# Kernel optimization log

Measured on AMD Instinct MI355X. Metric: run time of the kernel, lower is better.

Reference implementation:

```python
import jax, jax.numpy as jnp
import numpy as np

B, C, W, H = 32, 256, 64, 64
CQ = C // 4

def setup_inputs() -> dict:
    key = jax.random.key(0)
    ks = jax.random.split(key, 9)
    s = lambda fan: 1.0 / np.sqrt(fan)
    return {
        "x_0": jax.random.normal(ks[0], (B, C, W, H), jnp.float32),
        "x_1": jax.random.normal(ks[1], (B, C, W, H), jnp.float32),
        "Wq": jax.random.normal(ks[2], (CQ, C), jnp.float32) * s(C),
        "bq": jax.random.normal(ks[3], (CQ,), jnp.float32) * 0.01,
        "Wk": jax.random.normal(ks[4], (CQ, C), jnp.float32) * s(C),
        "bk": jax.random.normal(ks[5], (CQ,), jnp.float32) * 0.01,
        "Wv": jax.random.normal(ks[6], (C, C), jnp.float32) * s(C),
        "bv": jax.random.normal(ks[7], (C,), jnp.float32) * 0.01,
        "gamma": jax.random.normal(ks[8], (1,), jnp.float32) * 0.1,
    }

def reference(x_0, x_1, Wq, bq, Wk, bk, Wv, bv, gamma):
    # 1x1 convs == channel GEMMs
    q = jnp.einsum('oc,bchw->bohw', Wq, x_0) + bq[None, :, None, None]  # [B, C/4, W, H]
    k = jnp.einsum('oc,bchw->bohw', Wk, x_1) + bk[None, :, None, None]  # [B, C/4, W, H]
    v = jnp.einsum('oc,bchw->bohw', Wv, x_0) + bv[None, :, None, None]  # [B, C, W, H]
    b0 = x_0.shape[0]
    b1, c1, w1, h1 = x_1.shape
    proj_query = q.reshape(b0, -1).T            # [D, B0], D = (C/4)*W*H
    proj_key = k.reshape(b1, -1)                # [B1, D]
    energy = proj_key @ proj_query              # [B1, B0] attention over BATCH axis
    attention = jax.nn.softmax(energy, axis=-1)
    proj_value = v.reshape(b0, -1)              # [B0, C*W*H]
    out = (attention @ proj_value).reshape(b1, c1, w1, h1)
    out = gamma[0] * out + x_1
    return out, attention
```

## Files before the change

### kernel.cpp

```cpp
#include <hip/hip_runtime.h>

#define NB  32
#define NC  256
#define NCQ 64
#define WHT 4096
#define DQK ((size_t)NCQ * WHT)
#define MV  ((size_t)NC * WHT)

typedef __attribute__((ext_vector_type(8))) short short8;
typedef __attribute__((ext_vector_type(4))) float f32x4;
typedef __attribute__((ext_vector_type(2))) float f32x2;
typedef unsigned short ushort_t;

__device__ __forceinline__ ushort_t bf16_rne(float f) {
    union { float f; unsigned u; } v; v.f = f;
    unsigned r = (v.u + 0x7fffu + ((v.u >> 16) & 1u)) >> 16;
    return (ushort_t)r;
}
__device__ __forceinline__ float bf16_f(ushort_t h) {
    union { unsigned u; float f; } v; v.u = ((unsigned)h) << 16; return v.f;
}

__device__ __forceinline__ int frag_off(int r, int kk) {
    return ((kk >> 5) * 16 + ((kk >> 3) & 3) * 4 + (r >> 4)) * 128
           + (r & 15) * 8 + (kk & 7);
}

__global__ __launch_bounds__(256)
void prep_w(const float* __restrict__ Wq, const float* __restrict__ Wk,
            const float* __restrict__ Wv,
            ushort_t* __restrict__ wv_hi,
            ushort_t* __restrict__ wq_hi, ushort_t* __restrict__ wq_lo,
            ushort_t* __restrict__ wk_hi, ushort_t* __restrict__ wk_lo)
{
    int i = blockIdx.x * 256 + threadIdx.x;
    if (i < 65536) {
        int R = i >> 8, kk = i & 255;
        wv_hi[(R >> 6) * 16384 + frag_off(R & 63, kk)] = bf16_rne(Wv[i]);
    } else if (i < 81920) {
        int j = i - 65536; int r = j >> 8, kk = j & 255;
        float f = Wq[j]; ushort_t h = bf16_rne(f);
        int o = frag_off(r, kk);
        wq_hi[o] = h; wq_lo[o] = bf16_rne(f - bf16_f(h));
    } else if (i < 98304) {
        int j = i - 81920; int r = j >> 8, kk = j & 255;
        float f = Wk[j]; ushort_t h = bf16_rne(f);
        int o = frag_off(r, kk);
        wk_hi[o] = h; wk_lo[o] = bf16_rne(f - bf16_f(h));
    }
}

#define LOADB(dst, kbv) do {                                            \
    const float* xk_ = xw + (size_t)(kbv) * 32 * WHT;                   \
    _Pragma("unroll") for (int n_ = 0; n_ < 2; ++n_)                    \
    _Pragma("unroll") for (int e_ = 0; e_ < 8; ++e_)                    \
        dst[n_][e_] = xk_[(size_t)e_ * WHT + n_ * 16];                  \
} while (0)

__global__ __launch_bounds__(512, 4)
void qkv_mfma(const float* __restrict__ x0, const float* __restrict__ x1,
              const ushort_t* __restrict__ wv_hi,
              const ushort_t* __restrict__ wq_hi, const ushort_t* __restrict__ wq_lo,
              const ushort_t* __restrict__ wk_hi, const ushort_t* __restrict__ wk_lo,
              const float* __restrict__ bq, const float* __restrict__ bk,
              const float* __restrict__ bv,
              float* __restrict__ q, float* __restrict__ k,
              ushort_t* __restrict__ vbf)
{
    __shared__ ushort_t lds_hi[16384];
    __shared__ ushort_t lds_lo[16384];

    const int t   = threadIdx.x;
    const int bid = blockIdx.x;
    const int xcd = bid & 7;
    const int sl  = bid >> 3;
    const int mt  = sl % 6;
    const int g   = (sl / 6) * 8 + xcd;
    const int nt  = g & 15;
    const int b   = g >> 4;

    const bool isV = (mt < 4);
    const bool isQ = (mt == 4);

    const int wave = t >> 6;
    const int lane = t & 63;
    const int lh   = lane >> 4;
    const int ll   = lane & 15;

    const ushort_t* whi = isV ? (wv_hi + mt * 16384) : (isQ ? wq_hi : wk_hi);
    const ushort_t* wlo = isQ ? wq_lo : wk_lo;

#pragma unroll
    for (int r = 0; r < 4; ++r)
        *(short8*)&lds_hi[(r * 512 + t) * 8] = *(const short8*)(whi + (r * 512 + t) * 8);
    if (!isV) {
#pragma unroll
        for (int r = 0; r < 4; ++r)
            *(short8*)&lds_lo[(r * 512 + t) * 8] = *(const short8*)(wlo + (r * 512 + t) * 8);
    }
    __syncthreads();

    const float* xw = ((mt == 5) ? x1 : x0) + (size_t)b * NC * WHT
                      + nt * 256 + wave * 32 + ll + (size_t)lh * 8 * WHT;
    const int abase = lh * 512 + ll * 8;

    f32x4 acc[4][2];
#pragma unroll
    for (int m = 0; m < 4; ++m)
#pragma unroll
        for (int n = 0; n < 2; ++n) acc[m][n] = (f32x4){0.f, 0.f, 0.f, 0.f};

    float xfA[2][8], xfB[2][8];
    LOADB(xfA, 0);

#pragma unroll
    for (int kb = 0; kb < 8; ++kb) {
        float (*cur)[8] = (kb & 1) ? xfB : xfA;
        float (*nxt)[8] = (kb & 1) ? xfA : xfB;
        if (kb < 7) LOADB(nxt, kb + 1);

        short8 bh[2];
#pragma unroll
        for (int n = 0; n < 2; ++n) {
            union { unsigned u[4]; short8 s; } pk;
#pragma unroll
            for (int p = 0; p < 4; ++p)
                pk.u[p] = __builtin_amdgcn_perm(
                    __float_as_uint(cur[n][2 * p + 1]),
                    __float_as_uint(cur[n][2 * p]), 0x07060302u);
            bh[n] = pk.s;
        }

        if (isV) {
#pragma unroll
            for (int m = 0; m < 4; ++m) {
                short8 a_hi = *(const short8*)&lds_hi[kb * 2048 + abase + m * 128];
#pragma unroll
                for (int n = 0; n < 2; ++n)
                    acc[m][n] = __builtin_amdgcn_mfma_f32_16x16x32_bf16(
                        a_hi, bh[n], acc[m][n], 0, 0, 0);
            }
        } else {
            short8 bl[2];
#pragma unroll
            for (int n = 0; n < 2; ++n) {
                float lo[8];
#pragma unroll
                for (int e = 0; e < 8; ++e) {
                    float hf = __uint_as_float(__float_as_uint(cur[n][e]) & 0xffff0000u);
                    lo[e] = cur[n][e] - hf;
                }
                union { unsigned u[4]; short8 s; } pk;
#pragma unroll
                for (int p = 0; p < 4; ++p)
                    pk.u[p] = __builtin_amdgcn_perm(
                        __float_as_uint(lo[2 * p + 1]),
                        __float_as_uint(lo[2 * p]), 0x07060302u);
                bl[n] = pk.s;
            }
#pragma unroll
            for (int m = 0; m < 4; ++m) {
                short8 a_hi = *(const short8*)&lds_hi[kb * 2048 + abase + m * 128];
                short8 a_lo = *(const short8*)&lds_lo[kb * 2048 + abase + m * 128];
#pragma unroll
                for (int n = 0; n < 2; ++n) {
                    acc[m][n] = __builtin_amdgcn_mfma_f32_16x16x32_bf16(
                        a_hi, bh[n], acc[m][n], 0, 0, 0);
                    acc[m][n] = __builtin_amdgcn_mfma_f32_16x16x32_bf16(
                        a_hi, bl[n], acc[m][n], 0, 0, 0);
                    acc[m][n] = __builtin_amdgcn_mfma_f32_16x16x32_bf16(
                        a_lo, bh[n], acc[m][n], 0, 0, 0);
                }
            }
        }
    }

    const int colbase = nt * 256 + wave * 32;
    if (isV) {
        ushort_t* outp = vbf + ((size_t)b * NC + mt * 64) * WHT + colbase;
        const float* bias = bv + mt * 64;
#pragma unroll
        for (int m = 0; m < 4; ++m)
#pragma unroll
            for (int n = 0; n < 2; ++n)
#pragma unroll
                for (int r = 0; r < 4; ++r) {
                    const int row = m * 16 + 4 * lh + r;
                    outp[(size_t)row * WHT + n * 16 + ll] =
                        bf16_rne(acc[m][n][r] + bias[row]);
                }
    } else {
        float* outp = (isQ ? q : k) + (size_t)b * NCQ * WHT + colbase;
        const float* bias = isQ ? bq : bk;
#pragma unroll
        for (int m = 0; m < 4; ++m)
#pragma unroll
            for (int n = 0; n < 2; ++n)
#pragma unroll
                for (int r = 0; r < 4; ++r) {
                    const int row = m * 16 + 4 * lh + r;
                    outp[(size_t)row * WHT + n * 16 + ll] =
                        acc[m][n][r] + bias[row];
                }
    }
}

__global__ __launch_bounds__(256)
void energy_kernel(const float* __restrict__ q, const float* __restrict__ k,
                   float* __restrict__ energy)
{
    __shared__ float kt[256][17];
    __shared__ float qt[256][17];

    const int t  = threadIdx.x;
    const int d0 = blockIdx.x * 256;
    const int ih = blockIdx.y;
    const int jh = blockIdx.z;

    for (int r = 0; r < 16; ++r) {
        kt[t][r] = k[(size_t)(ih * 16 + r) * DQK + d0 + t];
        qt[t][r] = q[(size_t)(jh * 16 + r) * DQK + d0 + t];
    }
    __syncthreads();

    const int ii = t >> 4;
    const int jj = t & 15;
    float a0 = 0.f, a1 = 0.f, a2 = 0.f, a3 = 0.f;
#pragma unroll 8
    for (int d = 0; d < 256; d += 4) {
        a0 = fmaf(kt[d + 0][ii], qt[d + 0][jj], a0);
        a1 = fmaf(kt[d + 1][ii], qt[d + 1][jj], a1);
        a2 = fmaf(kt[d + 2][ii], qt[d + 2][jj], a2);
        a3 = fmaf(kt[d + 3][ii], qt[d + 3][jj], a3);
    }

    atomicAdd(&energy[(ih * 16 + ii) * 32 + jh * 16 + jj], (a0 + a1) + (a2 + a3));
}

__global__ __launch_bounds__(1024)
void softmax_kernel(const float* __restrict__ energy,
                    float* __restrict__ att, float* __restrict__ att_out)
{
    const int t = threadIdx.x;
    const int i = t >> 5;
    const int j = t & 31;
    float e = energy[i * 32 + j];
    float m = e;
#pragma unroll
    for (int o = 16; o; o >>= 1) m = fmaxf(m, __shfl_xor(m, o, 32));
    float ex = __expf(e - m);
    float s = ex;
#pragma unroll
    for (int o = 16; o; o >>= 1) s += __shfl_xor(s, o, 32);
    float a = ex / s;
    att[i * 32 + j] = a;
    att_out[i * 32 + j] = a;
}

__global__ __launch_bounds__(256)
void out_kernel(const ushort_t* __restrict__ vbf, const float* __restrict__ att,
                const float* __restrict__ x1, const float* __restrict__ gamma,
                float* __restrict__ out)
{
    const int t = threadIdx.x;
    const size_t m0 = (size_t)blockIdx.x * 512 + 2 * t;

    float v0[32], v1[32];
#pragma unroll
    for (int j = 0; j < 32; ++j) {
        unsigned u = *(const unsigned*)(vbf + (size_t)j * MV + m0);
        v0[j] = __uint_as_float(u << 16);
        v1[j] = __uint_as_float(u & 0xffff0000u);
    }

    const float g = gamma[0];
    for (int i = 0; i < 32; ++i) {
        float a0 = 0.f, a1 = 0.f;
#pragma unroll
        for (int j = 0; j < 32; ++j) {
            float w = att[i * 32 + j];
            a0 = fmaf(w, v0[j], a0);
            a1 = fmaf(w, v1[j], a1);
        }
        f32x2 xx = *(const f32x2*)(x1 + (size_t)i * MV + m0);
        f32x2 oo; oo.x = g * a0 + xx.x; oo.y = g * a1 + xx.y;
        *(f32x2*)(out + (size_t)i * MV + m0) = oo;
    }
}

extern "C" void kernel_launch(void* const* d_in, const int* in_sizes, int n_in,
                              void* d_out, int out_size, void* d_ws, size_t ws_size,
                              hipStream_t stream)
{
    const float* x0    = (const float*)d_in[0];
    const float* x1    = (const float*)d_in[1];
    const float* Wq    = (const float*)d_in[2];
    const float* bq    = (const float*)d_in[3];
    const float* Wk    = (const float*)d_in[4];
    const float* bk    = (const float*)d_in[5];
    const float* Wv    = (const float*)d_in[6];
    const float* bv    = (const float*)d_in[7];
    const float* gamma = (const float*)d_in[8];

    float* ws     = (float*)d_ws;
    float* q      = ws;
    float* k      = q + (size_t)NB * NCQ * WHT;
    float* energy = k + (size_t)NB * NCQ * WHT;
    float* att    = energy + 1024;

    ushort_t* wv_hi = (ushort_t*)(att + 1024);
    ushort_t* wq_hi = wv_hi + 65536;
    ushort_t* wq_lo = wq_hi + 16384;
    ushort_t* wk_hi = wq_lo + 16384;
    ushort_t* wk_lo = wk_hi + 16384;
    ushort_t* vbf   = wk_lo + 16384;

    float* out     = (float*)d_out;
    float* att_out = out + (size_t)NB * NC * WHT;

    hipMemsetAsync(energy, 0, 1024 * sizeof(float), stream);

    prep_w<<<384, 256, 0, stream>>>(Wq, Wk, Wv, wv_hi, wq_hi, wq_lo, wk_hi, wk_lo);
    qkv_mfma<<<3072, 512, 0, stream>>>(x0, x1, wv_hi, wq_hi, wq_lo, wk_hi, wk_lo,
                                       bq, bk, bv, q, k, vbf);
    energy_kernel<<<dim3(1024, 2, 2), 256, 0, stream>>>(q, k, energy);
    softmax_kernel<<<1, 1024, 0, stream>>>(energy, att, att_out);
    out_kernel<<<2048, 256, 0, stream>>>(vbf, att, x1, gamma, out);
}
```

Baseline: 246.0 us.

## Split Q/K projection blocks in half, drop lo LDS, add explicit pipelining

Q and K tiles were the slow blocks because each does three MFMAs per product on the same work as a V tile. This change splits each Q and K tile across two blocks handling 128 columns each, which raises the grid from 3072 to 4096 blocks and balances per-block work. The lo weight fragments are now read straight from global memory instead of a second LDS buffer, which halves LDS use. The double-buffered loads are restructured with sched_barriers to control interleaving. The risks are extra global traffic for the lo weights and more block launches.

```diff
diff --git a/kernel.cpp b/kernel.cpp
--- a/kernel.cpp
+++ b/kernel.cpp
@@ -50,12 +50,59 @@
     }
 }
 
-#define LOADB(dst, kbv) do {                                            \
+#define PACK_HI(dst, src) do {                                          \
+    union { unsigned u[4]; short8 s; } pk_;                             \
+    _Pragma("unroll") for (int p_ = 0; p_ < 4; ++p_)                    \
+        pk_.u[p_] = __builtin_amdgcn_perm(                              \
+            __float_as_uint(src[2 * p_ + 1]),                           \
+            __float_as_uint(src[2 * p_]), 0x07060302u);                 \
+    dst = pk_.s;                                                        \
+} while (0)
+
+#define LOADB2(dst, kbv) do {                                           \
     const float* xk_ = xw + (size_t)(kbv) * 32 * WHT;                   \
     _Pragma("unroll") for (int n_ = 0; n_ < 2; ++n_)                    \
     _Pragma("unroll") for (int e_ = 0; e_ < 8; ++e_)                    \
         dst[n_][e_] = xk_[(size_t)e_ * WHT + n_ * 16];                  \
 } while (0)
+
+#define LOADB1(dst, kbv) do {                                           \
+    const float* xk_ = xw + (size_t)(kbv) * 32 * WHT;                   \
+    _Pragma("unroll") for (int e_ = 0; e_ < 8; ++e_)                    \
+        dst[e_] = xk_[(size_t)e_ * WHT];                                \
+} while (0)
+
+#define PROCV(buf, kbv) do {                                            \
+    short8 bh_[2];                                                      \
+    _Pragma("unroll") for (int n_ = 0; n_ < 2; ++n_)                    \
+        PACK_HI(bh_[n_], buf[n_]);                                      \
+    _Pragma("unroll") for (int m_ = 0; m_ < 4; ++m_) {                  \
+        short8 ah_ = *(const short8*)&lds_hi[(kbv) * 2048 + abase + m_ * 128]; \
+        _Pragma("unroll") for (int n_ = 0; n_ < 2; ++n_)                \
+            acc[m_][n_] = __builtin_amdgcn_mfma_f32_16x16x32_bf16(      \
+                ah_, bh_[n_], acc[m_][n_], 0, 0, 0);                    \
+    }                                                                   \
+} while (0)
+
+#define PROCQK(buf, kbv) do {                                           \
+    short8 bh_, bl_;                                                    \
+    PACK_HI(bh_, buf);                                                  \
+    float lo_[8];                                                       \
+    _Pragma("unroll") for (int e_ = 0; e_ < 8; ++e_) {                  \
+        float hf_ = __uint_as_float(__float_as_uint(buf[e_]) & 0xffff0000u); \
+        lo_[e_] = buf[e_] - hf_;                                        \
+    }                                                                   \
+    PACK_HI(bl_, lo_);                                                  \
+    _Pragma("unroll") for (int m_ = 0; m_ < 4; ++m_) {                  \
+        short8 ah_ = *(const short8*)&lds_hi[(kbv) * 2048 + abase + m_ * 128]; \
+        short8 al_ = *(const short8*)(wlo + (kbv) * 2048 + abase + m_ * 128);  \
+        acc2[m_] = __builtin_amdgcn_mfma_f32_16x16x32_bf16(ah_, bh_, acc2[m_], 0, 0, 0); \
+        acc2[m_] = __builtin_amdgcn_mfma_f32_16x16x32_bf16(ah_, bl_, acc2[m_], 0, 0, 0); \
+        acc2[m_] = __builtin_amdgcn_mfma_f32_16x16x32_bf16(al_, bh_, acc2[m_], 0, 0, 0); \
+    }                                                                   \
+} while (0)
+
+#define SBAR() __builtin_amdgcn_sched_barrier(0)
 
 __global__ __launch_bounds__(512, 4)
 void qkv_mfma(const float* __restrict__ x0, const float* __restrict__ x1,
@@ -68,117 +115,61 @@
               ushort_t* __restrict__ vbf)
 {
     __shared__ ushort_t lds_hi[16384];
-    __shared__ ushort_t lds_lo[16384];
 
     const int t   = threadIdx.x;
     const int bid = blockIdx.x;
-    const int xcd = bid & 7;
-    const int sl  = bid >> 3;
-    const int mt  = sl % 6;
-    const int g   = (sl / 6) * 8 + xcd;
-    const int nt  = g & 15;
-    const int b   = g >> 4;
-
-    const bool isV = (mt < 4);
-    const bool isQ = (mt == 4);
+    const int xcd  = bid & 7;
+    const int r0   = bid >> 3;
+    const int slot = r0 & 7;
+    const int gg   = r0 >> 3;
+    const int g    = gg * 8 + xcd;
+    const int nt   = g & 15;
+    const int b    = g >> 4;
+
+    const bool isV = (slot < 4);
 
     const int wave = t >> 6;
     const int lane = t & 63;
     const int lh   = lane >> 4;
     const int ll   = lane & 15;
 
-    const ushort_t* whi = isV ? (wv_hi + mt * 16384) : (isQ ? wq_hi : wk_hi);
-    const ushort_t* wlo = isQ ? wq_lo : wk_lo;
+    const ushort_t* whi = isV ? (wv_hi + slot * 16384)
+                              : ((slot < 6) ? wq_hi : wk_hi);
 
 #pragma unroll
     for (int r = 0; r < 4; ++r)
         *(short8*)&lds_hi[(r * 512 + t) * 8] = *(const short8*)(whi + (r * 512 + t) * 8);
-    if (!isV) {
-#pragma unroll
-        for (int r = 0; r < 4; ++r)
-            *(short8*)&lds_lo[(r * 512 + t) * 8] = *(const short8*)(wlo + (r * 512 + t) * 8);
-    }
     __syncthreads();
 
-    const float* xw = ((mt == 5) ? x1 : x0) + (size_t)b * NC * WHT
-                      + nt * 256 + wave * 32 + ll + (size_t)lh * 8 * WHT;
     const int abase = lh * 512 + ll * 8;
 
-    f32x4 acc[4][2];
-#pragma unroll
-    for (int m = 0; m < 4; ++m)
-#pragma unroll
-        for (int n = 0; n < 2; ++n) acc[m][n] = (f32x4){0.f, 0.f, 0.f, 0.f};
-
-    float xfA[2][8], xfB[2][8];
-    LOADB(xfA, 0);
-
-#pragma unroll
-    for (int kb = 0; kb < 8; ++kb) {
-        float (*cur)[8] = (kb & 1) ? xfB : xfA;
-        float (*nxt)[8] = (kb & 1) ? xfA : xfB;
-        if (kb < 7) LOADB(nxt, kb + 1);
-
-        short8 bh[2];
-#pragma unroll
-        for (int n = 0; n < 2; ++n) {
-            union { unsigned u[4]; short8 s; } pk;
-#pragma unroll
-            for (int p = 0; p < 4; ++p)
-                pk.u[p] = __builtin_amdgcn_perm(
-                    __float_as_uint(cur[n][2 * p + 1]),
-                    __float_as_uint(cur[n][2 * p]), 0x07060302u);
-            bh[n] = pk.s;
+    if (isV) {
+        const float* xw = x0 + (size_t)b * NC * WHT
+                          + nt * 256 + wave * 32 + ll + (size_t)lh * 8 * WHT;
+
+        f32x4 acc[4][2];
+#pragma unroll
+        for (int m = 0; m < 4; ++m)
+#pragma unroll
+            for (int n = 0; n < 2; ++n) acc[m][n] = (f32x4){0.f, 0.f, 0.f, 0.f};
+
+        float xfA[2][8], xfB[2][8];
+        LOADB2(xfA, 0);
+        SBAR();
+#pragma unroll
+        for (int p = 0; p < 4; ++p) {
+            LOADB2(xfB, 2 * p + 1);
+            SBAR();
+            PROCV(xfA, 2 * p);
+            if (p < 3) LOADB2(xfA, 2 * p + 2);
+            SBAR();
+            PROCV(xfB, 2 * p + 1);
+            SBAR();
         }
 
-        if (isV) {
-#pragma unroll
-            for (int m = 0; m < 4; ++m) {
-                short8 a_hi = *(const short8*)&lds_hi[kb * 2048 + abase + m * 128];
-#pragma unroll
-                for (int n = 0; n < 2; ++n)
-                    acc[m][n] = __builtin_amdgcn_mfma_f32_16x16x32_bf16(
-                        a_hi, bh[n], acc[m][n], 0, 0, 0);
-            }
-        } else {
-            short8 bl[2];
-#pragma unroll
-            for (int n = 0; n < 2; ++n) {
-                float lo[8];
-#pragma unroll
-                for (int e = 0; e < 8; ++e) {
-                    float hf = __uint_as_float(__float_as_uint(cur[n][e]) & 0xffff0000u);
-                    lo[e] = cur[n][e] - hf;
-                }
-                union { unsigned u[4]; short8 s; } pk;
-#pragma unroll
-                for (int p = 0; p < 4; ++p)
-                    pk.u[p] = __builtin_amdgcn_perm(
-                        __float_as_uint(lo[2 * p + 1]),
-                        __float_as_uint(lo[2 * p]), 0x07060302u);
-                bl[n] = pk.s;
-            }
-#pragma unroll
-            for (int m = 0; m < 4; ++m) {
-                short8 a_hi = *(const short8*)&lds_hi[kb * 2048 + abase + m * 128];
-                short8 a_lo = *(const short8*)&lds_lo[kb * 2048 + abase + m * 128];
-#pragma unroll
-                for (int n = 0; n < 2; ++n) {
-                    acc[m][n] = __builtin_amdgcn_mfma_f32_16x16x32_bf16(
-                        a_hi, bh[n], acc[m][n], 0, 0, 0);
-                    acc[m][n] = __builtin_amdgcn_mfma_f32_16x16x32_bf16(
-                        a_hi, bl[n], acc[m][n], 0, 0, 0);
-                    acc[m][n] = __builtin_amdgcn_mfma_f32_16x16x32_bf16(
-                        a_lo, bh[n], acc[m][n], 0, 0, 0);
-                }
-            }
-        }
-    }
-
-    const int colbase = nt * 256 + wave * 32;
-    if (isV) {
-        ushort_t* outp = vbf + ((size_t)b * NC + mt * 64) * WHT + colbase;
-        const float* bias = bv + mt * 64;
+        const int colbase = nt * 256 + wave * 32;
+        ushort_t* outp = vbf + ((size_t)b * NC + slot * 64) * WHT + colbase;
+        const float* bias = bv + slot * 64;
 #pragma unroll
         for (int m = 0; m < 4; ++m)
 #pragma unroll
@@ -190,18 +181,42 @@
                         bf16_rne(acc[m][n][r] + bias[row]);
                 }
     } else {
+        const bool isQ  = (slot < 6);
+        const int  half = slot & 1;
+        const ushort_t* wlo = isQ ? wq_lo : wk_lo;
+
+        const float* xw = (isQ ? x0 : x1) + (size_t)b * NC * WHT
+                          + nt * 256 + half * 128 + wave * 16 + ll
+                          + (size_t)lh * 8 * WHT;
+
+        f32x4 acc2[4];
+#pragma unroll
+        for (int m = 0; m < 4; ++m) acc2[m] = (f32x4){0.f, 0.f, 0.f, 0.f};
+
+        float xfA[8], xfB[8];
+        LOADB1(xfA, 0);
+        SBAR();
+#pragma unroll
+        for (int p = 0; p < 4; ++p) {
+            LOADB1(xfB, 2 * p + 1);
+            SBAR();
+            PROCQK(xfA, 2 * p);
+            if (p < 3) LOADB1(xfA, 2 * p + 2);
+            SBAR();
+            PROCQK(xfB, 2 * p + 1);
+            SBAR();
+        }
+
+        const int colbase = nt * 256 + half * 128 + wave * 16;
         float* outp = (isQ ? q : k) + (size_t)b * NCQ * WHT + colbase;
         const float* bias = isQ ? bq : bk;
 #pragma unroll
         for (int m = 0; m < 4; ++m)
 #pragma unroll
-            for (int n = 0; n < 2; ++n)
-#pragma unroll
-                for (int r = 0; r < 4; ++r) {
-                    const int row = m * 16 + 4 * lh + r;
-                    outp[(size_t)row * WHT + n * 16 + ll] =
-                        acc[m][n][r] + bias[row];
-                }
+            for (int r = 0; r < 4; ++r) {
+                const int row = m * 16 + 4 * lh + r;
+                outp[(size_t)row * WHT + ll] = acc2[m][r] + bias[row];
+            }
     }
 }
 
@@ -321,7 +336,7 @@
     hipMemsetAsync(energy, 0, 1024 * sizeof(float), stream);
 
     prep_w<<<384, 256, 0, stream>>>(Wq, Wk, Wv, wv_hi, wq_hi, wq_lo, wk_hi, wk_lo);
-    qkv_mfma<<<3072, 512, 0, stream>>>(x0, x1, wv_hi, wq_hi, wq_lo, wk_hi, wk_lo,
+    qkv_mfma<<<4096, 512, 0, stream>>>(x0, x1, wv_hi, wq_hi, wq_lo, wk_hi, wk_lo,
                                        bq, bk, bv, q, k, vbf);
     energy_kernel<<<dim3(1024, 2, 2), 256, 0, stream>>>(q, k, energy);
     softmax_kernel<<<1, 1024, 0, stream>>>(energy, att, att_out);
```

Measured after the change: 264.3 us. +7.4%, slower.

## Stage X panels via global_load_lds and fuse softmax into output kernel

Applied to the files above, without the earlier changes.

The QKV projection kernel now streams activation panels into double-buffered LDS with asynchronous global-to-LDS loads and reads the bf16 weight fragments straight from global memory, where before the weights sat in LDS and activations went direct to registers. This is meant to coalesce the strided activation reads and overlap them with MFMA work, at the cost of a barrier per k-step and uncached weight loads from global. Separately, the single-block softmax kernel is removed: every output block recomputes the 32x32 softmax into shared memory and block 0 writes the attention output, saving a launch and a round trip through global memory in exchange for redundant softmax work.

```diff
diff --git a/kernel.cpp b/kernel.cpp
--- a/kernel.cpp
+++ b/kernel.cpp
@@ -24,6 +24,12 @@
 __device__ __forceinline__ int frag_off(int r, int kk) {
     return ((kk >> 5) * 16 + ((kk >> 3) & 3) * 4 + (r >> 4)) * 128
            + (r & 15) * 8 + (kk & 7);
+}
+
+__device__ __forceinline__ void gload_lds16(const float* g, float* l) {
+    __builtin_amdgcn_global_load_lds(
+        (const __attribute__((address_space(1))) unsigned*)g,
+        (__attribute__((address_space(3))) unsigned*)l, 16, 0, 0);
 }
 
 __global__ __launch_bounds__(256)
@@ -50,11 +56,27 @@
     }
 }
 
-#define LOADB(dst, kbv) do {                                            \
-    const float* xk_ = xw + (size_t)(kbv) * 32 * WHT;                   \
+#define PACK_HI(dst, src) do {                                          \
+    union { unsigned u[4]; short8 s; } pk_;                             \
+    _Pragma("unroll") for (int p_ = 0; p_ < 4; ++p_)                    \
+        pk_.u[p_] = __builtin_amdgcn_perm(                              \
+            __float_as_uint(src[2 * p_ + 1]),                           \
+            __float_as_uint(src[2 * p_]), 0x07060302u);                 \
+    dst = pk_.s;                                                        \
+} while (0)
+
+#define STAGE(bufi, kbv) do {                                           \
+    _Pragma("unroll") for (int r_ = 0; r_ < 4; ++r_) {                  \
+        const int ch_ = wave * 4 + r_;                                  \
+        gload_lds16(xpanel + (size_t)((kbv) * 32 + ch_) * WHT + (lane << 2), \
+                    &Xl[bufi][ch_][0]);                                 \
+    }                                                                   \
+} while (0)
+
+#define LOADXF(xf, cur) do {                                            \
     _Pragma("unroll") for (int n_ = 0; n_ < 2; ++n_)                    \
     _Pragma("unroll") for (int e_ = 0; e_ < 8; ++e_)                    \
-        dst[n_][e_] = xk_[(size_t)e_ * WHT + n_ * 16];                  \
+        xf[n_][e_] = Xl[cur][lh * 8 + e_][spb + n_ * 16];               \
 } while (0)
 
 __global__ __launch_bounds__(512, 4)
@@ -67,8 +89,7 @@
               float* __restrict__ q, float* __restrict__ k,
               ushort_t* __restrict__ vbf)
 {
-    __shared__ ushort_t lds_hi[16384];
-    __shared__ ushort_t lds_lo[16384];
+    __shared__ float Xl[2][32][256];
 
     const int t   = threadIdx.x;
     const int bid = blockIdx.x;
@@ -87,22 +108,12 @@
     const int lh   = lane >> 4;
     const int ll   = lane & 15;
 
+    const float* xpanel = ((mt == 5) ? x1 : x0) + (size_t)b * NC * WHT + nt * 256;
     const ushort_t* whi = isV ? (wv_hi + mt * 16384) : (isQ ? wq_hi : wk_hi);
     const ushort_t* wlo = isQ ? wq_lo : wk_lo;
 
-#pragma unroll
-    for (int r = 0; r < 4; ++r)
-        *(short8*)&lds_hi[(r * 512 + t) * 8] = *(const short8*)(whi + (r * 512 + t) * 8);
-    if (!isV) {
-#pragma unroll
-        for (int r = 0; r < 4; ++r)
-            *(short8*)&lds_lo[(r * 512 + t) * 8] = *(const short8*)(wlo + (r * 512 + t) * 8);
-    }
-    __syncthreads();
-
-    const float* xw = ((mt == 5) ? x1 : x0) + (size_t)b * NC * WHT
-                      + nt * 256 + wave * 32 + ll + (size_t)lh * 8 * WHT;
     const int abase = lh * 512 + ll * 8;
+    const int spb   = wave * 32 + ll;
 
     f32x4 acc[4][2];
 #pragma unroll
@@ -110,73 +121,35 @@
 #pragma unroll
         for (int n = 0; n < 2; ++n) acc[m][n] = (f32x4){0.f, 0.f, 0.f, 0.f};
 
-    float xfA[2][8], xfB[2][8];
-    LOADB(xfA, 0);
-
-#pragma unroll
-    for (int kb = 0; kb < 8; ++kb) {
-        float (*cur)[8] = (kb & 1) ? xfB : xfA;
-        float (*nxt)[8] = (kb & 1) ? xfA : xfB;
-        if (kb < 7) LOADB(nxt, kb + 1);
-
-        short8 bh[2];
-#pragma unroll
-        for (int n = 0; n < 2; ++n) {
-            union { unsigned u[4]; short8 s; } pk;
-#pragma unroll
-            for (int p = 0; p < 4; ++p)
-                pk.u[p] = __builtin_amdgcn_perm(
-                    __float_as_uint(cur[n][2 * p + 1]),
-                    __float_as_uint(cur[n][2 * p]), 0x07060302u);
-            bh[n] = pk.s;
-        }
-
-        if (isV) {
+    STAGE(0, 0);
+
+    if (isV) {
+#pragma unroll
+        for (int kb = 0; kb < 8; ++kb) {
+            asm volatile("s_waitcnt vmcnt(0)" ::: "memory");
+            __syncthreads();
+            if (kb < 7) STAGE((kb + 1) & 1, kb + 1);
+            __builtin_amdgcn_sched_barrier(0);
+
+            const int cur = kb & 1;
+            float xf[2][8];
+            LOADXF(xf, cur);
+
+            short8 bh[2];
+#pragma unroll
+            for (int n = 0; n < 2; ++n) PACK_HI(bh[n], xf[n]);
+
 #pragma unroll
             for (int m = 0; m < 4; ++m) {
-                short8 a_hi = *(const short8*)&lds_hi[kb * 2048 + abase + m * 128];
+                short8 ah = *(const short8*)(whi + kb * 2048 + abase + m * 128);
 #pragma unroll
                 for (int n = 0; n < 2; ++n)
                     acc[m][n] = __builtin_amdgcn_mfma_f32_16x16x32_bf16(
-                        a_hi, bh[n], acc[m][n], 0, 0, 0);
-            }
-        } else {
-            short8 bl[2];
-#pragma unroll
-            for (int n = 0; n < 2; ++n) {
-                float lo[8];
-#pragma unroll
-                for (int e = 0; e < 8; ++e) {
-                    float hf = __uint_as_float(__float_as_uint(cur[n][e]) & 0xffff0000u);
-                    lo[e] = cur[n][e] - hf;
-                }
-                union { unsigned u[4]; short8 s; } pk;
-#pragma unroll
-                for (int p = 0; p < 4; ++p)
-                    pk.u[p] = __builtin_amdgcn_perm(
-                        __float_as_uint(lo[2 * p + 1]),
-                        __float_as_uint(lo[2 * p]), 0x07060302u);
-                bl[n] = pk.s;
-            }
-#pragma unroll
-            for (int m = 0; m < 4; ++m) {
-                short8 a_hi = *(const short8*)&lds_hi[kb * 2048 + abase + m * 128];
-                short8 a_lo = *(const short8*)&lds_lo[kb * 2048 + abase + m * 128];
-#pragma unroll
-                for (int n = 0; n < 2; ++n) {
-                    acc[m][n] = __builtin_amdgcn_mfma_f32_16x16x32_bf16(
-                        a_hi, bh[n], acc[m][n], 0, 0, 0);
-                    acc[m][n] = __builtin_amdgcn_mfma_f32_16x16x32_bf16(
-                        a_hi, bl[n], acc[m][n], 0, 0, 0);
-                    acc[m][n] = __builtin_amdgcn_mfma_f32_16x16x32_bf16(
-                        a_lo, bh[n], acc[m][n], 0, 0, 0);
-                }
+                        ah, bh[n], acc[m][n], 0, 0, 0);
             }
         }
-    }
-
-    const int colbase = nt * 256 + wave * 32;
-    if (isV) {
+
+        const int colbase = nt * 256 + wave * 32;
         ushort_t* outp = vbf + ((size_t)b * NC + mt * 64) * WHT + colbase;
         const float* bias = bv + mt * 64;
 #pragma unroll
@@ -190,6 +163,47 @@
                         bf16_rne(acc[m][n][r] + bias[row]);
                 }
     } else {
+#pragma unroll
+        for (int kb = 0; kb < 8; ++kb) {
+            asm volatile("s_waitcnt vmcnt(0)" ::: "memory");
+            __syncthreads();
+            if (kb < 7) STAGE((kb + 1) & 1, kb + 1);
+            __builtin_amdgcn_sched_barrier(0);
+
+            const int cur = kb & 1;
+            float xf[2][8];
+            LOADXF(xf, cur);
+
+            short8 bh[2], bl[2];
+#pragma unroll
+            for (int n = 0; n < 2; ++n) {
+                PACK_HI(bh[n], xf[n]);
+                float lo[8];
+#pragma unroll
+                for (int e = 0; e < 8; ++e) {
+                    float hf = __uint_as_float(__float_as_uint(xf[n][e]) & 0xffff0000u);
+                    lo[e] = xf[n][e] - hf;
+                }
+                PACK_HI(bl[n], lo);
+            }
+
+#pragma unroll
+            for (int m = 0; m < 4; ++m) {
+                short8 ah = *(const short8*)(whi + kb * 2048 + abase + m * 128);
+                short8 al = *(const short8*)(wlo + kb * 2048 + abase + m * 128);
+#pragma unroll
+                for (int n = 0; n < 2; ++n) {
+                    acc[m][n] = __builtin_amdgcn_mfma_f32_16x16x32_bf16(
+                        ah, bh[n], acc[m][n], 0, 0, 0);
+                    acc[m][n] = __builtin_amdgcn_mfma_f32_16x16x32_bf16(
+                        ah, bl[n], acc[m][n], 0, 0, 0);
+                    acc[m][n] = __builtin_amdgcn_mfma_f32_16x16x32_bf16(
+                        al, bh[n], acc[m][n], 0, 0, 0);
+                }
+            }
+        }
+
+        const int colbase = nt * 256 + wave * 32;
         float* outp = (isQ ? q : k) + (size_t)b * NCQ * WHT + colbase;
         const float* bias = isQ ? bq : bk;
 #pragma unroll
@@ -237,32 +251,32 @@
     atomicAdd(&energy[(ih * 16 + ii) * 32 + jh * 16 + jj], (a0 + a1) + (a2 + a3));
 }
 
-__global__ __launch_bounds__(1024)
-void softmax_kernel(const float* __restrict__ energy,
-                    float* __restrict__ att, float* __restrict__ att_out)
-{
+__global__ __launch_bounds__(256)
+void out_kernel(const ushort_t* __restrict__ vbf, const float* __restrict__ energy,
+                const float* __restrict__ x1, const float* __restrict__ gamma,
+                float* __restrict__ out, float* __restrict__ att_out)
+{
+    __shared__ float att_s[1024];
     const int t = threadIdx.x;
-    const int i = t >> 5;
-    const int j = t & 31;
-    float e = energy[i * 32 + j];
-    float m = e;
-#pragma unroll
-    for (int o = 16; o; o >>= 1) m = fmaxf(m, __shfl_xor(m, o, 32));
-    float ex = __expf(e - m);
-    float s = ex;
-#pragma unroll
-    for (int o = 16; o; o >>= 1) s += __shfl_xor(s, o, 32);
-    float a = ex / s;
-    att[i * 32 + j] = a;
-    att_out[i * 32 + j] = a;
-}
-
-__global__ __launch_bounds__(256)
-void out_kernel(const ushort_t* __restrict__ vbf, const float* __restrict__ att,
-                const float* __restrict__ x1, const float* __restrict__ gamma,
-                float* __restrict__ out)
-{
-    const int t = threadIdx.x;
+
+    if (t < 32) {
+        float e[32];
+        float m = -1e30f;
+#pragma unroll
+        for (int j = 0; j < 32; ++j) { e[j] = energy[t * 32 + j]; m = fmaxf(m, e[j]); }
+        float s = 0.f;
+#pragma unroll
+        for (int j = 0; j < 32; ++j) { e[j] = __expf(e[j] - m); s += e[j]; }
+        float inv = 1.f / s;
+#pragma unroll
+        for (int j = 0; j < 32; ++j) att_s[t * 32 + j] = e[j] * inv;
+    }
+    __syncthreads();
+
+    if (blockIdx.x == 0) {
+        for (int r = t; r < 1024; r += 256) att_out[r] = att_s[r];
+    }
+
     const size_t m0 = (size_t)blockIdx.x * 512 + 2 * t;
 
     float v0[32], v1[32];
@@ -278,7 +292,7 @@
         float a0 = 0.f, a1 = 0.f;
 #pragma unroll
         for (int j = 0; j < 32; ++j) {
-            float w = att[i * 32 + j];
+            float w = att_s[i * 32 + j];
             a0 = fmaf(w, v0[j], a0);
             a1 = fmaf(w, v1[j], a1);
         }
@@ -306,9 +320,8 @@
     float* q      = ws;
     float* k      = q + (size_t)NB * NCQ * WHT;
     float* energy = k + (size_t)NB * NCQ * WHT;
-    float* att    = energy + 1024;
-
-    ushort_t* wv_hi = (ushort_t*)(att + 1024);
+
+    ushort_t* wv_hi = (ushort_t*)(energy + 1024);
     ushort_t* wq_hi = wv_hi + 65536;
     ushort_t* wq_lo = wq_hi + 16384;
     ushort_t* wk_hi = wq_lo + 16384;
@@ -324,6 +337,5 @@
     qkv_mfma<<<3072, 512, 0, stream>>>(x0, x1, wv_hi, wq_hi, wq_lo, wk_hi, wk_lo,
                                        bq, bk, bv, q, k, vbf);
     energy_kernel<<<dim3(1024, 2, 2), 256, 0, stream>>>(q, k, energy);
-    softmax_kernel<<<1, 1024, 0, stream>>>(energy, att, att_out);
-    out_kernel<<<2048, 256, 0, stream>>>(vbf, att, x1, gamma, out);
-}
+    out_kernel<<<2048, 256, 0, stream>>>(vbf, energy, x1, gamma, out, att_out);
+}
```

After: 271.3 us. +10.3%, slower.

## Restructure energy kernel to full 32x32 tiles and fuse softmax into output kernel

Applied to the files above, without the earlier changes.

The energy kernel now has each block compute the full 32x32 K·Q tile over a 512-wide slice of D, staged in 128-wide chunks. Each thread accumulates two outputs. This cuts the q/k reads from four blocks per slice to one and reduces the number of atomic adds. The separate softmax launch is removed: every out_kernel block recomputes the 32x32 softmax from energy into shared memory, and block 0 writes the attention output. This saves a launch and a global round trip, at the cost of redundant softmax work per block. An unused PACK_HI macro is also added.

```diff
diff --git a/kernel.cpp b/kernel.cpp
--- a/kernel.cpp
+++ b/kernel.cpp
@@ -57,6 +57,15 @@
         dst[n_][e_] = xk_[(size_t)e_ * WHT + n_ * 16];                  \
 } while (0)
 
+#define PACK_HI(dst, src) do {                                          \
+    union { unsigned u[4]; short8 s; } pk_;                             \
+    _Pragma("unroll") for (int p_ = 0; p_ < 4; ++p_)                    \
+        pk_.u[p_] = __builtin_amdgcn_perm(                              \
+            __float_as_uint(src[2 * p_ + 1]),                           \
+            __float_as_uint(src[2 * p_]), 0x07060302u);                 \
+    dst = pk_.s;                                                        \
+} while (0)
+
 __global__ __launch_bounds__(512, 4)
 void qkv_mfma(const float* __restrict__ x0, const float* __restrict__ x1,
               const ushort_t* __restrict__ wv_hi,
@@ -205,64 +214,77 @@
     }
 }
 
-__global__ __launch_bounds__(256)
+__global__ __launch_bounds__(512)
 void energy_kernel(const float* __restrict__ q, const float* __restrict__ k,
                    float* __restrict__ energy)
 {
-    __shared__ float kt[256][17];
-    __shared__ float qt[256][17];
-
-    const int t  = threadIdx.x;
-    const int d0 = blockIdx.x * 256;
-    const int ih = blockIdx.y;
-    const int jh = blockIdx.z;
-
-    for (int r = 0; r < 16; ++r) {
-        kt[t][r] = k[(size_t)(ih * 16 + r) * DQK + d0 + t];
-        qt[t][r] = q[(size_t)(jh * 16 + r) * DQK + d0 + t];
+    __shared__ float kt[32][129];
+    __shared__ float qt[32][129];
+
+    const int t   = threadIdx.x;
+    const int d00 = blockIdx.x * 512;
+    const int i   = t >> 4;
+    const int j   = t & 15;
+
+    float a0 = 0.f, a1 = 0.f, a2 = 0.f, a3 = 0.f;
+    float b0 = 0.f, b1 = 0.f, b2 = 0.f, b3 = 0.f;
+
+    for (int c = 0; c < 4; ++c) {
+        const int d0 = d00 + c * 128;
+        __syncthreads();
+#pragma unroll
+        for (int u = 0; u < 8; ++u) {
+            int idx = u * 512 + t;
+            int ii = idx >> 7, d = idx & 127;
+            kt[ii][d] = k[(size_t)ii * DQK + d0 + d];
+            qt[ii][d] = q[(size_t)ii * DQK + d0 + d];
+        }
+        __syncthreads();
+
+#pragma unroll 4
+        for (int d = 0; d < 128; d += 4) {
+            float k0 = kt[i][d], k1 = kt[i][d + 1], k2 = kt[i][d + 2], k3 = kt[i][d + 3];
+            a0 = fmaf(k0, qt[j][d],      a0);
+            a1 = fmaf(k1, qt[j][d + 1],  a1);
+            a2 = fmaf(k2, qt[j][d + 2],  a2);
+            a3 = fmaf(k3, qt[j][d + 3],  a3);
+            b0 = fmaf(k0, qt[j + 16][d],     b0);
+            b1 = fmaf(k1, qt[j + 16][d + 1], b1);
+            b2 = fmaf(k2, qt[j + 16][d + 2], b2);
+            b3 = fmaf(k3, qt[j + 16][d + 3], b3);
+        }
+    }
+
+    atomicAdd(&energy[i * 32 + j],      (a0 + a1) + (a2 + a3));
+    atomicAdd(&energy[i * 32 + j + 16], (b0 + b1) + (b2 + b3));
+}
+
+__global__ __launch_bounds__(256)
+void out_kernel(const ushort_t* __restrict__ vbf, const float* __restrict__ energy,
+                const float* __restrict__ x1, const float* __restrict__ gamma,
+                float* __restrict__ out, float* __restrict__ att_out)
+{
+    __shared__ float att_s[1024];
+    const int t = threadIdx.x;
+
+    if (t < 32) {
+        float e[32];
+        float m = -1e30f;
+#pragma unroll
+        for (int j = 0; j < 32; ++j) { e[j] = energy[t * 32 + j]; m = fmaxf(m, e[j]); }
+        float s = 0.f;
+#pragma unroll
+        for (int j = 0; j < 32; ++j) { e[j] = __expf(e[j] - m); s += e[j]; }
+        float inv = 1.f / s;
+#pragma unroll
+        for (int j = 0; j < 32; ++j) att_s[t * 32 + j] = e[j] * inv;
     }
     __syncthreads();
 
-    const int ii = t >> 4;
-    const int jj = t & 15;
-    float a0 = 0.f, a1 = 0.f, a2 = 0.f, a3 = 0.f;
-#pragma unroll 8
-    for (int d = 0; d < 256; d += 4) {
-        a0 = fmaf(kt[d + 0][ii], qt[d + 0][jj], a0);
-        a1 = fmaf(kt[d + 1][ii], qt[d + 1][jj], a1);
-        a2 = fmaf(kt[d + 2][ii], qt[d + 2][jj], a2);
-        a3 = fmaf(kt[d + 3][ii], qt[d + 3][jj], a3);
-    }
-
-    atomicAdd(&energy[(ih * 16 + ii) * 32 + jh * 16 + jj], (a0 + a1) + (a2 + a3));
-}
-
-__global__ __launch_bounds__(1024)
-void softmax_kernel(const float* __restrict__ energy,
-                    float* __restrict__ att, float* __restrict__ att_out)
-{
-    const int t = threadIdx.x;
-    const int i = t >> 5;
-    const int j = t & 31;
-    float e = energy[i * 32 + j];
-    float m = e;
-#pragma unroll
-    for (int o = 16; o; o >>= 1) m = fmaxf(m, __shfl_xor(m, o, 32));
-    float ex = __expf(e - m);
-    float s = ex;
-#pragma unroll
-    for (int o = 16; o; o >>= 1) s += __shfl_xor(s, o, 32);
-    float a = ex / s;
-    att[i * 32 + j] = a;
-    att_out[i * 32 + j] = a;
-}
-
-__global__ __launch_bounds__(256)
-void out_kernel(const ushort_t* __restrict__ vbf, const float* __restrict__ att,
-                const float* __restrict__ x1, const float* __restrict__ gamma,
-                float* __restrict__ out)
-{
-    const int t = threadIdx.x;
+    if (blockIdx.x == 0) {
+        for (int r = t; r < 1024; r += 256) att_out[r] = att_s[r];
+    }
+
     const size_t m0 = (size_t)blockIdx.x * 512 + 2 * t;
 
     float v0[32], v1[32];
@@ -278,7 +300,7 @@
         float a0 = 0.f, a1 = 0.f;
 #pragma unroll
         for (int j = 0; j < 32; ++j) {
-            float w = att[i * 32 + j];
+            float w = att_s[i * 32 + j];
             a0 = fmaf(w, v0[j], a0);
             a1 = fmaf(w, v1[j], a1);
         }
@@ -306,9 +328,8 @@
     float* q      = ws;
     float* k      = q + (size_t)NB * NCQ * WHT;
     float* energy = k + (size_t)NB * NCQ * WHT;
-    float* att    = energy + 1024;
-
-    ushort_t* wv_hi = (ushort_t*)(att + 1024);
+
+    ushort_t* wv_hi = (ushort_t*)(energy + 1024);
     ushort_t* wq_hi = wv_hi + 65536;
     ushort_t* wq_lo = wq_hi + 16384;
     ushort_t* wk_hi = wq_lo + 16384;
@@ -323,7 +344,6 @@
     prep_w<<<384, 256, 0, stream>>>(Wq, Wk, Wv, wv_hi, wq_hi, wq_lo, wk_hi, wk_lo);
     qkv_mfma<<<3072, 512, 0, stream>>>(x0, x1, wv_hi, wq_hi, wq_lo, wk_hi, wk_lo,
                                        bq, bk, bv, q, k, vbf);
-    energy_kernel<<<dim3(1024, 2, 2), 256, 0, stream>>>(q, k, energy);
-    softmax_kernel<<<1, 1024, 0, stream>>>(energy, att, att_out);
-    out_kernel<<<2048, 256, 0, stream>>>(vbf, att, x1, gamma, out);
-}
+    energy_kernel<<<512, 512, 0, stream>>>(q, k, energy);
+    out_kernel<<<2048, 256, 0, stream>>>(vbf, energy, x1, gamma, out, att_out);
+}
```

Measured after the change: 225.8 us. -8.2%, faster.
